# Performance work log

Measured on AMD Instinct MI355X. Metric: run time of the kernel, lower is better.

## Reference

```python
import jax, jax.numpy as jnp
import numpy as np

HIDDEN = 1024
HEADS = 16
HEAD_DIM = HIDDEN // HEADS


def setup_inputs() -> dict:
    key = jax.random.key(0)
    ks = jax.random.split(key, 12)
    B, S, D = 2, 2048, HIDDEN
    scale = 1.0 / np.sqrt(D)
    return {
        "query": jax.random.normal(ks[0], (B, S, D), jnp.float32),
        "key": jax.random.normal(ks[1], (B, S, D), jnp.float32),
        "value": jax.random.normal(ks[2], (B, S, D), jnp.float32),
        "Wq": jax.random.normal(ks[3], (D, D), jnp.float32) * scale,
        "bq": jnp.zeros((D,), jnp.float32),
        "Wk": jax.random.normal(ks[4], (D, D), jnp.float32) * scale,
        "bk": jnp.zeros((D,), jnp.float32),
        "Wv": jax.random.normal(ks[5], (D, D), jnp.float32) * scale,
        "bv": jnp.zeros((D,), jnp.float32),
        "Wo": jax.random.normal(ks[6], (D, D), jnp.float32) * scale,
        "bo": jnp.zeros((D,), jnp.float32),
    }


def reference(query, key, value, Wq, bq, Wk, bk, Wv, bv, Wo, bo):
    B, S, D = query.shape
    H, Hd = HEADS, HEAD_DIM
    sm_scale = 1.0 / jnp.sqrt(jnp.asarray(Hd, query.dtype))

    def proj(x, W, b):  # nn.Linear: x @ W.T + b, then split heads -> [B,H,S,Hd]
        y = jnp.einsum("bsd,ed->bse", x, W) + b
        return y.reshape(B, S, H, Hd).transpose(0, 2, 1, 3)

    Q = proj(query, Wq, bq)
    K = proj(key, Wk, bk)
    V = proj(value, Wv, bv)

    scores = jnp.einsum("bhqd,bhkd->bhqk", Q, K) * sm_scale  # [B,H,S,S]
    attn = jax.nn.softmax(scores, axis=-1)
    ctx = jnp.einsum("bhqk,bhkd->bhqd", attn, V)
    ctx = ctx.transpose(0, 2, 1, 3).reshape(B, S, D)
    out = jnp.einsum("bsd,ed->bse", ctx, Wo) + bo
    return out
```

## Files before the change

### kernel.cpp

```cpp
#include <hip/hip_runtime.h>
#include <stdint.h>

typedef unsigned short u16;
typedef unsigned int u32;
typedef __attribute__((ext_vector_type(8))) short s16x8;
typedef __attribute__((ext_vector_type(4))) float fx4;

#define AS_GLOBAL __attribute__((address_space(1)))
#define AS_LDS    __attribute__((address_space(3)))

__device__ __forceinline__ void g2l16(const u16* g, u16* l) {
  __builtin_amdgcn_global_load_lds((const AS_GLOBAL unsigned int*)g,
                                   (AS_LDS unsigned int*)l, 16, 0, 0);
}
__device__ __forceinline__ u16 f2bf(float f) {
  u32 u = __float_as_uint(f);
  u += 0x7FFF + ((u >> 16) & 1);
  return (u16)(u >> 16);
}
__device__ __forceinline__ u32 pkcvt(float a, float b) {
  u32 r;
  asm("v_cvt_pk_bf16_f32 %0, %1, %2" : "=v"(r) : "v"(a), "v"(b));
  return r;
}

__global__ __launch_bounds__(256) void cvt3(const float* __restrict__ a, const float* __restrict__ b,
                                            const float* __restrict__ c, u16* oa, u16* ob, u16* oc, int n4) {
  const float* src = blockIdx.y == 0 ? a : blockIdx.y == 1 ? b : c;
  u16* dst = blockIdx.y == 0 ? oa : blockIdx.y == 1 ? ob : oc;
  int i = blockIdx.x * 256 + threadIdx.x;
  if (i >= n4) return;
  float4 f = ((const float4*)src)[i];
  ushort4 o; o.x = f2bf(f.x); o.y = f2bf(f.y); o.z = f2bf(f.z); o.w = f2bf(f.w);
  ((ushort4*)dst)[i] = o;
}
__global__ __launch_bounds__(256) void cvt4(const float* __restrict__ a, const float* __restrict__ b,
                                            const float* __restrict__ c, const float* __restrict__ d,
                                            u16* oa, u16* ob, u16* oc, u16* od, int n4) {
  const float* src = blockIdx.y == 0 ? a : blockIdx.y == 1 ? b : blockIdx.y == 2 ? c : d;
  u16* dst = blockIdx.y == 0 ? oa : blockIdx.y == 1 ? ob : blockIdx.y == 2 ? oc : od;
  int i = blockIdx.x * 256 + threadIdx.x;
  if (i >= n4) return;
  float4 f = ((const float4*)src)[i];
  ushort4 o; o.x = f2bf(f.x); o.y = f2bf(f.y); o.z = f2bf(f.z); o.w = f2bf(f.w);
  ((ushort4*)dst)[i] = o;
}

__global__ __launch_bounds__(256) void gemm_qkv(
    const u16* __restrict__ Aq, const u16* __restrict__ Ak, const u16* __restrict__ Av,
    const u16* __restrict__ Wq, const u16* __restrict__ Wk, const u16* __restrict__ Wv,
    const float* __restrict__ bq, const float* __restrict__ bk, const float* __restrict__ bv,
    u16* __restrict__ Oq, u16* __restrict__ Ok, u16* __restrict__ Ovt)
{
  constexpr int K = 1024;
  __shared__ u16 As[128 * 32];
  __shared__ u16 Bs[128 * 32];
  const int z = blockIdx.z;
  const u16* A = z == 0 ? Aq : z == 1 ? Ak : Av;
  const u16* W = z == 0 ? Wq : z == 1 ? Wk : Wv;
  const float* bias = z == 0 ? bq : z == 1 ? bk : bv;
  const float scale = z == 0 ? 0.180336880f : 1.0f;

  const int bm = blockIdx.x, bn = blockIdx.y;
  const int tid = threadIdx.x;
  const int lane = tid & 63, wave = tid >> 6;
  const int quad = lane >> 4, col = lane & 15;
  const int wm = wave >> 1, wn = wave & 1;

  const int L0 = tid, L1 = 256 + tid;
  const int r0 = L0 >> 2, c0 = (L0 & 3) ^ ((r0 >> 1) & 3);
  const int r1 = L1 >> 2, c1 = (L1 & 3) ^ ((r1 >> 1) & 3);
  const u16* gA0 = A + (bm * 128 + r0) * K + c0 * 8;
  const u16* gA1 = A + (bm * 128 + r1) * K + c1 * 8;
  const u16* gB0 = W + (bn * 128 + r0) * K + c0 * 8;
  const u16* gB1 = W + (bn * 128 + r1) * K + c1 * 8;
  u16* lA0 = As + L0 * 8; u16* lA1 = As + L1 * 8;
  u16* lB0 = Bs + L0 * 8; u16* lB1 = Bs + L1 * 8;

  const int aRow = wm * 64 + col;
  const int bRow = wn * 64 + col;

  fx4 zero = {0.f, 0.f, 0.f, 0.f};
  fx4 acc[4][4];
#pragma unroll
  for (int i = 0; i < 4; ++i)
#pragma unroll
    for (int j = 0; j < 4; ++j) acc[i][j] = zero;

  for (int kb = 0; kb < K / 32; ++kb) {
    __syncthreads();
    g2l16(gA0 + kb * 32, lA0);
    g2l16(gA1 + kb * 32, lA1);
    g2l16(gB0 + kb * 32, lB0);
    g2l16(gB1 + kb * 32, lB1);
    __syncthreads();
    s16x8 af[4], bf[4];
#pragma unroll
    for (int mt = 0; mt < 4; ++mt) {
      int row = aRow + mt * 16;
      int ch = row * 4 + (quad ^ ((row >> 1) & 3));
      af[mt] = *(const s16x8*)(As + ch * 8);
    }
#pragma unroll
    for (int nt = 0; nt < 4; ++nt) {
      int row = bRow + nt * 16;
      int ch = row * 4 + (quad ^ ((row >> 1) & 3));
      bf[nt] = *(const s16x8*)(Bs + ch * 8);
    }
#pragma unroll
    for (int mt = 0; mt < 4; ++mt)
#pragma unroll
      for (int nt = 0; nt < 4; ++nt)
        acc[mt][nt] = __builtin_amdgcn_mfma_f32_16x16x32_bf16(af[mt], bf[nt], acc[mt][nt], 0, 0, 0);
  }

  if (z == 2) {
#pragma unroll
    for (int nt = 0; nt < 4; ++nt) {
      int n = bn * 128 + wn * 64 + nt * 16 + col;
      float bvv = bias[n];
      int h = n >> 6, hd = n & 63;
#pragma unroll
      for (int mt = 0; mt < 4; ++mt) {
        int mbase = bm * 128 + wm * 64 + mt * 16 + quad * 4;
        int b = mbase >> 11, s = mbase & 2047;
        uint2 w;
        w.x = pkcvt(acc[mt][nt][0] + bvv, acc[mt][nt][1] + bvv);
        w.y = pkcvt(acc[mt][nt][2] + bvv, acc[mt][nt][3] + bvv);
        *(uint2*)(Ovt + ((size_t)((b * 16 + h) * 64 + hd)) * 2048 + s) = w;
      }
    }
  } else {
    u16* outB = z == 0 ? Oq : Ok;
#pragma unroll
    for (int nt = 0; nt < 4; ++nt) {
      int n = bn * 128 + wn * 64 + nt * 16 + col;
      float bvv = bias[n];
#pragma unroll
      for (int mt = 0; mt < 4; ++mt) {
        int mbase = bm * 128 + wm * 64 + mt * 16 + quad * 4;
#pragma unroll
        for (int reg = 0; reg < 4; ++reg) {
          int m = mbase + reg;
          float v = (acc[mt][nt][reg] + bvv) * scale;
          int b = m >> 11, s = m & 2047;
          int h = n >> 6, hd = n & 63;
          outB[((b * 16 + h) * 2048 + s) * 64 + hd] = f2bf(v);
        }
      }
    }
  }
}

__global__ __launch_bounds__(256) void gemm_out(
    const u16* __restrict__ A, const u16* __restrict__ W,
    const float* __restrict__ bias, float* __restrict__ outF)
{
  constexpr int K = 1024;
  __shared__ u16 As[128 * 32];
  __shared__ u16 Bs[64 * 32];
  const int bm = blockIdx.x, bn = blockIdx.y;
  const int tid = threadIdx.x;
  const int lane = tid & 63, wave = tid >> 6;
  const int quad = lane >> 4, col = lane & 15;
  const int wm = wave >> 1, wn = wave & 1;

  const int L0 = tid, L1 = 256 + tid;
  const int r0 = L0 >> 2, c0 = (L0 & 3) ^ ((r0 >> 1) & 3);
  const int r1 = L1 >> 2, c1 = (L1 & 3) ^ ((r1 >> 1) & 3);
  const u16* gA0 = A + (bm * 128 + r0) * K + c0 * 8;
  const u16* gA1 = A + (bm * 128 + r1) * K + c1 * 8;
  const u16* gB0 = W + (bn * 64 + r0) * K + c0 * 8;
  u16* lA0 = As + L0 * 8; u16* lA1 = As + L1 * 8;
  u16* lB0 = Bs + L0 * 8;

  const int aRow = wm * 64 + col;
  const int bRow = wn * 32 + col;

  fx4 zero = {0.f, 0.f, 0.f, 0.f};
  fx4 acc[4][2];
#pragma unroll
  for (int i = 0; i < 4; ++i)
#pragma unroll
    for (int j = 0; j < 2; ++j) acc[i][j] = zero;

  for (int kb = 0; kb < K / 32; ++kb) {
    __syncthreads();
    g2l16(gA0 + kb * 32, lA0);
    g2l16(gA1 + kb * 32, lA1);
    g2l16(gB0 + kb * 32, lB0);
    __syncthreads();
    s16x8 af[4], bf[2];
#pragma unroll
    for (int mt = 0; mt < 4; ++mt) {
      int row = aRow + mt * 16;
      int ch = row * 4 + (quad ^ ((row >> 1) & 3));
      af[mt] = *(const s16x8*)(As + ch * 8);
    }
#pragma unroll
    for (int nt = 0; nt < 2; ++nt) {
      int row = bRow + nt * 16;
      int ch = row * 4 + (quad ^ ((row >> 1) & 3));
      bf[nt] = *(const s16x8*)(Bs + ch * 8);
    }
#pragma unroll
    for (int mt = 0; mt < 4; ++mt)
#pragma unroll
      for (int nt = 0; nt < 2; ++nt)
        acc[mt][nt] = __builtin_amdgcn_mfma_f32_16x16x32_bf16(af[mt], bf[nt], acc[mt][nt], 0, 0, 0);
  }

#pragma unroll
  for (int nt = 0; nt < 2; ++nt) {
    int n = bn * 64 + wn * 32 + nt * 16 + col;
    float bvv = bias[n];
#pragma unroll
    for (int mt = 0; mt < 4; ++mt) {
      int mbase = bm * 128 + wm * 64 + mt * 16 + quad * 4;
#pragma unroll
      for (int reg = 0; reg < 4; ++reg)
        outF[(mbase + reg) * 1024 + n] = acc[mt][nt][reg] + bvv;
    }
  }
}

__global__ __launch_bounds__(256, 4) void flash_attn(
    const u16* __restrict__ Qp, const u16* __restrict__ Kp,
    const u16* __restrict__ Vt, u16* __restrict__ ctx)
{
  __shared__ u16 sh[16384];
  const int qt = blockIdx.x, bh = blockIdx.y;
  const int tid = threadIdx.x, lane = tid & 63, wave = tid >> 6;
  const int quad = lane >> 4, col = lane & 15;
  const int wm = wave >> 1, wn = wave & 1;

  const u16* Qb = Qp + ((size_t)bh * 2048 + qt * 64) * 64;
  const u16* Kb = Kp + (size_t)bh * 2048 * 64;
  const u16* Vb = Vt + (size_t)bh * 64 * 2048;

  s16x8 qf[2][2];
#pragma unroll
  for (int mt = 0; mt < 2; ++mt)
#pragma unroll
    for (int h = 0; h < 2; ++h)
      qf[mt][h] = *(const s16x8*)(Qb + (wm * 32 + mt * 16 + col) * 64 + h * 32 + quad * 8);

  fx4 zero = {0.f, 0.f, 0.f, 0.f};
  fx4 acc_o[2][4], acc_l[2];
#pragma unroll
  for (int mt = 0; mt < 2; ++mt) {
    acc_l[mt] = zero;
#pragma unroll
    for (int dt = 0; dt < 4; ++dt) acc_o[mt][dt] = zero;
  }
  s16x8 ones;
#pragma unroll
  for (int j = 0; j < 8; ++j) ones[j] = (short)0x3F80;

  u16* Vs = sh;
  u16* Pw = sh + 8192 + wave * 2048;

  s16x8 kf0[4], kf1[4];
  auto loadK = [&](int kvi) {
#pragma unroll
    for (int nt = 0; nt < 4; ++nt) {
      const u16* kr = Kb + (kvi * 128 + wn * 64 + nt * 16 + col) * 64 + quad * 8;
      kf0[nt] = *(const s16x8*)(kr);
      kf1[nt] = *(const s16x8*)(kr + 32);
    }
  };
  loadK(0);

  const u16* vsrc[4];
#pragma unroll
  for (int i = 0; i < 4; ++i) {
    int d = wave * 16 + i * 4 + (lane >> 4);
    int cs = (lane & 15) ^ (d & 15);
    vsrc[i] = Vb + d * 2048 + cs * 8;
  }

  for (int kv = 0; kv < 16; ++kv) {
    const int n0 = kv * 128;
    __builtin_amdgcn_s_barrier();
#pragma unroll
    for (int i = 0; i < 4; ++i)
      g2l16(vsrc[i] + n0, Vs + (wave * 16 + i * 4) * 128);

    __builtin_amdgcn_s_setprio(1);
#pragma unroll
    for (int nt = 0; nt < 4; ++nt) {
#pragma unroll
      for (int mt = 0; mt < 2; ++mt) {
        fx4 s = __builtin_amdgcn_mfma_f32_16x16x32_bf16(kf0[nt], qf[mt][0], zero, 0, 0, 0);
        s = __builtin_amdgcn_mfma_f32_16x16x32_bf16(kf1[nt], qf[mt][1], s, 0, 0, 0);
        int m = mt * 16 + col;
        int cch = 2 * nt + (quad >> 1);
        uint2 w;
        w.x = pkcvt(exp2f(s[0]), exp2f(s[1]));
        w.y = pkcvt(exp2f(s[2]), exp2f(s[3]));
        *(uint2*)(Pw + m * 64 + ((cch ^ (m & 7))) * 8 + (quad & 1) * 4) = w;
      }
    }
    __builtin_amdgcn_s_setprio(0);

    asm volatile("s_waitcnt vmcnt(0)" ::: "memory");
    loadK((kv + 1) & 15);
    asm volatile("s_waitcnt lgkmcnt(0)" ::: "memory");
    __builtin_amdgcn_s_barrier();

    __builtin_amdgcn_s_setprio(1);
#pragma unroll
    for (int ks = 0; ks < 2; ++ks) {
      s16x8 pf[2];
#pragma unroll
      for (int mt = 0; mt < 2; ++mt)
        pf[mt] = *(const s16x8*)(Pw + (mt * 16 + col) * 64 + ((4 * ks + quad) ^ (col & 7)) * 8);
#pragma unroll
      for (int dt = 0; dt < 4; ++dt) {
        s16x8 vf = *(const s16x8*)(Vs + (dt * 16 + col) * 128 + ((wn * 8 + 4 * ks + quad) ^ col) * 8);
#pragma unroll
        for (int mt = 0; mt < 2; ++mt)
          acc_o[mt][dt] = __builtin_amdgcn_mfma_f32_16x16x32_bf16(pf[mt], vf, acc_o[mt][dt], 0, 0, 0);
      }
#pragma unroll
      for (int mt = 0; mt < 2; ++mt)
        acc_l[mt] = __builtin_amdgcn_mfma_f32_16x16x32_bf16(pf[mt], ones, acc_l[mt], 0, 0, 0);
    }
    __builtin_amdgcn_s_setprio(0);
  }

  __syncthreads();
  float* buf = (float*)sh;
  if (wn == 1) {
#pragma unroll
    for (int mt = 0; mt < 2; ++mt) {
#pragma unroll
      for (int dt = 0; dt < 4; ++dt)
#pragma unroll
        for (int e = 0; e < 4; ++e)
          buf[wm * 2560 + ((mt * 4 + dt) * 4 + e) * 64 + lane] = acc_o[mt][dt][e];
#pragma unroll
      for (int e = 0; e < 4; ++e)
        buf[wm * 2560 + (32 + mt * 4 + e) * 64 + lane] = acc_l[mt][e];
    }
  }
  __syncthreads();
  if (wn == 0) {
    const int b = bh >> 4, h = bh & 15;
#pragma unroll
    for (int mt = 0; mt < 2; ++mt) {
      fx4 rl;
#pragma unroll
      for (int e = 0; e < 4; ++e) {
        float l = acc_l[mt][e] + buf[wm * 2560 + (32 + mt * 4 + e) * 64 + lane];
        rl[e] = 1.0f / l;
      }
#pragma unroll
      for (int dt = 0; dt < 4; ++dt)
#pragma unroll
        for (int e = 0; e < 4; ++e) {
          float v = (acc_o[mt][dt][e] + buf[wm * 2560 + ((mt * 4 + dt) * 4 + e) * 64 + lane]) * rl[e];
          int s = qt * 64 + wm * 32 + mt * 16 + quad * 4 + e;
          ctx[((size_t)(b * 2048 + s)) * 1024 + h * 64 + dt * 16 + col] = f2bf(v);
        }
    }
  }
}

extern "C" void kernel_launch(void* const* d_in, const int* in_sizes, int n_in,
                              void* d_out, int out_size, void* d_ws, size_t ws_size,
                              hipStream_t stream) {
  const float* q  = (const float*)d_in[0];
  const float* k  = (const float*)d_in[1];
  const float* v  = (const float*)d_in[2];
  const float* Wq = (const float*)d_in[3];
  const float* bq = (const float*)d_in[4];
  const float* Wk = (const float*)d_in[5];
  const float* bk = (const float*)d_in[6];
  const float* Wv = (const float*)d_in[7];
  const float* bv = (const float*)d_in[8];
  const float* Wo = (const float*)d_in[9];
  const float* bo = (const float*)d_in[10];
  float* out = (float*)d_out;

  char* ws = (char*)d_ws;
  const size_t MB = 1u << 20;
  u16* qb  = (u16*)(ws + 0 * MB);
  u16* kb  = (u16*)(ws + 8 * MB);
  u16* vb  = (u16*)(ws + 16 * MB);
  u16* wqb = (u16*)(ws + 24 * MB);
  u16* wkb = (u16*)(ws + 26 * MB);
  u16* wvb = (u16*)(ws + 28 * MB);
  u16* wob = (u16*)(ws + 30 * MB);
  u16* Qp  = (u16*)(ws + 32 * MB);
  u16* Kp  = (u16*)(ws + 40 * MB);
  u16* Vtp = (u16*)(ws + 56 * MB);
  u16* ctx = (u16*)(ws + 64 * MB);

  cvt3<<<dim3(4096, 3), 256, 0, stream>>>(q, k, v, qb, kb, vb, 1048576);
  cvt4<<<dim3(1024, 4), 256, 0, stream>>>(Wq, Wk, Wv, Wo, wqb, wkb, wvb, wob, 262144);

  gemm_qkv<<<dim3(32, 8, 3), 256, 0, stream>>>(qb, kb, vb, wqb, wkb, wvb,
                                               bq, bk, bv, Qp, Kp, Vtp);
  flash_attn<<<dim3(32, 32), 256, 0, stream>>>(Qp, Kp, Vtp, ctx);
  gemm_out<<<dim3(32, 16), 256, 0, stream>>>(ctx, wob, bo, out);
}
```

Measured before the change: 255.3 us.

## Stage K tiles through LDS via async global-to-LDS loads instead of registers

K tiles are now copied into a swizzled LDS buffer with global_load_lds, prefetched during the PV phase, and read from LDS for the QK MFMAs. Before, each wave loaded its K fragments straight into registers. The change is meant to cut register pressure and overlap K fetches with compute. It raises LDS use to 48KB per block and lowers the occupancy hint from 4 to 3 blocks. It also adds a vmcnt wait at the end of each iteration, which can stall on the K load.

```diff
diff --git a/kernel.cpp b/kernel.cpp
--- a/kernel.cpp
+++ b/kernel.cpp
@@ -224,11 +224,11 @@
   }
 }
 
-__global__ __launch_bounds__(256, 4) void flash_attn(
+__global__ __launch_bounds__(256, 3) void flash_attn(
     const u16* __restrict__ Qp, const u16* __restrict__ Kp,
     const u16* __restrict__ Vt, u16* __restrict__ ctx)
 {
-  __shared__ u16 sh[16384];
+  __shared__ u16 sh[24576];
   const int qt = blockIdx.x, bh = blockIdx.y;
   const int tid = threadIdx.x, lane = tid & 63, wave = tid >> 6;
   const int quad = lane >> 4, col = lane & 15;
@@ -258,18 +258,8 @@
   for (int j = 0; j < 8; ++j) ones[j] = (short)0x3F80;
 
   u16* Vs = sh;
-  u16* Pw = sh + 8192 + wave * 2048;
-
-  s16x8 kf0[4], kf1[4];
-  auto loadK = [&](int kvi) {
-#pragma unroll
-    for (int nt = 0; nt < 4; ++nt) {
-      const u16* kr = Kb + (kvi * 128 + wn * 64 + nt * 16 + col) * 64 + quad * 8;
-      kf0[nt] = *(const s16x8*)(kr);
-      kf1[nt] = *(const s16x8*)(kr + 32);
-    }
-  };
-  loadK(0);
+  u16* Ks = sh + 8192;
+  u16* Pw = sh + 16384 + wave * 2048;
 
   const u16* vsrc[4];
 #pragma unroll
@@ -279,6 +269,20 @@
     vsrc[i] = Vb + d * 2048 + cs * 8;
   }
 
+  const u16* ksrc[4];
+  u16* kdst[4];
+#pragma unroll
+  for (int i = 0; i < 4; ++i) {
+    int idx = wave * 256 + i * 64 + lane;
+    int d = idx >> 3, c = idx & 7;
+    ksrc[i] = Kb + d * 64 + (c ^ (d & 7)) * 8;
+    kdst[i] = Ks + (wave * 256 + i * 64) * 8;
+  }
+
+#pragma unroll
+  for (int i = 0; i < 4; ++i) g2l16(ksrc[i], kdst[i]);
+  asm volatile("s_waitcnt vmcnt(0)" ::: "memory");
+
   for (int kv = 0; kv < 16; ++kv) {
     const int n0 = kv * 128;
     __builtin_amdgcn_s_barrier();
@@ -289,10 +293,15 @@
     __builtin_amdgcn_s_setprio(1);
 #pragma unroll
     for (int nt = 0; nt < 4; ++nt) {
+      const int r = wn * 64 + nt * 16 + col;
+      const u16* krow = Ks + r * 64;
+      const int x = r & 7;
+      s16x8 k0 = *(const s16x8*)(krow + ((quad ^ x) << 3));
+      s16x8 k1 = *(const s16x8*)(krow + (((4 ^ quad) ^ x) << 3));
 #pragma unroll
       for (int mt = 0; mt < 2; ++mt) {
-        fx4 s = __builtin_amdgcn_mfma_f32_16x16x32_bf16(kf0[nt], qf[mt][0], zero, 0, 0, 0);
-        s = __builtin_amdgcn_mfma_f32_16x16x32_bf16(kf1[nt], qf[mt][1], s, 0, 0, 0);
+        fx4 s = __builtin_amdgcn_mfma_f32_16x16x32_bf16(k0, qf[mt][0], zero, 0, 0, 0);
+        s = __builtin_amdgcn_mfma_f32_16x16x32_bf16(k1, qf[mt][1], s, 0, 0, 0);
         int m = mt * 16 + col;
         int cch = 2 * nt + (quad >> 1);
         uint2 w;
@@ -304,9 +313,14 @@
     __builtin_amdgcn_s_setprio(0);
 
     asm volatile("s_waitcnt vmcnt(0)" ::: "memory");
-    loadK((kv + 1) & 15);
     asm volatile("s_waitcnt lgkmcnt(0)" ::: "memory");
     __builtin_amdgcn_s_barrier();
+
+    if (kv < 15) {
+#pragma unroll
+      for (int i = 0; i < 4; ++i)
+        g2l16(ksrc[i] + (kv + 1) * 8192, kdst[i]);
+    }
 
     __builtin_amdgcn_s_setprio(1);
 #pragma unroll
@@ -327,6 +341,8 @@
         acc_l[mt] = __builtin_amdgcn_mfma_f32_16x16x32_bf16(pf[mt], ones, acc_l[mt], 0, 0, 0);
     }
     __builtin_amdgcn_s_setprio(0);
+
+    asm volatile("s_waitcnt vmcnt(0)" ::: "memory");
   }
 
   __syncthreads();
```

After: 232.7 us. 8.9% less time.
